# Kernel tuning notes

Measured on AMD Instinct MI355X. Metric: run time of the kernel, lower is better.

The kernel has to match this reference:

```python
import jax, jax.numpy as jnp
import numpy as np

NUM_NODES = 50000
NUM_RELS = 256
D = 256            # node_in_feat
TEXT_D = 256       # text_emb_dim
T_TOTAL = 24       # number of unique timestep graphs
E = 20000          # edges per timestep graph
B = 16             # batch of query times
SEQ_LEN = 7


def setup_inputs() -> dict:
    key = jax.random.key(0)
    ks = jax.random.split(key, 12)
    s = 1.0 / np.sqrt(D)
    return {
        "node_embeds": jax.random.normal(ks[0], (NUM_NODES, D), jnp.float32),
        "text_emb": jax.random.normal(ks[1], (T_TOTAL, E, TEXT_D), jnp.float32),
        "text_w_W": jax.random.uniform(ks[2], (TEXT_D, D), jnp.float32, -s, s),
        "text_w_b": jax.random.uniform(ks[3], (D,), jnp.float32, -s, s),
        "edge_w_W": jax.random.uniform(ks[4], (3 * D, D), jnp.float32, -s, s),
        "edge_w_b": jax.random.uniform(ks[5], (D,), jnp.float32, -s, s),
        "gru_Wih": jax.random.uniform(ks[6], (D, 3 * D), jnp.float32, -s, s),
        "gru_Whh": jax.random.uniform(ks[7], (D, 3 * D), jnp.float32, -s, s),
        "gru_bih": jax.random.uniform(ks[8], (3 * D,), jnp.float32, -s, s),
        "gru_bhh": jax.random.uniform(ks[9], (3 * D,), jnp.float32, -s, s),
        "edge_src": jax.random.randint(ks[10], (T_TOTAL, E), 0, NUM_NODES, jnp.int32),
        "edge_dst": jax.random.randint(jax.random.fold_in(ks[10], 1), (T_TOTAL, E), 0, NUM_NODES, jnp.int32),
        "edge_rel": jax.random.randint(jax.random.fold_in(ks[10], 2), (T_TOTAL, E), 0, NUM_RELS, jnp.int32),
        "time_idx": jax.random.randint(ks[11], (B, SEQ_LEN), 0, T_TOTAL, jnp.int32),
    }


def _gru(seqs, Wih, Whh, bih, bhh):
    # seqs: [B, R, S, d] -> run GRU over S, return final hidden [B, R, d]
    xs = jnp.moveaxis(seqs, 2, 0)  # [S, B, R, d]
    h0 = jnp.zeros(seqs.shape[:2] + (seqs.shape[-1],), seqs.dtype)

    def step(h, x):
        gi = x @ Wih + bih            # [B, R, 3d]
        gh = h @ Whh + bhh
        i_r, i_z, i_n = jnp.split(gi, 3, axis=-1)
        h_r, h_z, h_n = jnp.split(gh, 3, axis=-1)
        r = jax.nn.sigmoid(i_r + h_r)
        z = jax.nn.sigmoid(i_z + h_z)
        n = jnp.tanh(i_n + r * h_n)
        h_new = (1.0 - z) * n + z * h
        return h_new, None

    h_final, _ = jax.lax.scan(step, h0, xs)
    return h_final


def reference(node_embeds, text_emb, text_w_W, text_w_b, edge_w_W, edge_w_b,
              gru_Wih, gru_Whh, gru_bih, gru_bhh,
              edge_src, edge_dst, edge_rel, time_idx):
    # edge text projection (text_w): [T, E, D]
    text_h = text_emb @ text_w_W + text_w_b
    # gather node embeddings per edge endpoint
    h_src = node_embeds[edge_src]  # [T, E, D]
    h_dst = node_embeds[edge_dst]  # [T, E, D]
    # concat + edge MLP + ReLU: e_h = relu(edge_w([src || text || dst]))
    e = jnp.concatenate([h_src, text_h, h_dst], axis=-1)  # [T, E, 3D]
    e_h = jax.nn.relu(e @ edge_w_W + edge_w_b)            # [T, E, D]

    # scatter-mean of edge embeddings by relation type per timestep graph;
    # relations absent in a graph get zeros (init_rel_embeds = zeros)
    seg = lambda v, r: jax.ops.segment_sum(v, r, num_segments=NUM_RELS)
    sums = jax.vmap(seg)(e_h, edge_rel)                               # [T, R, D]
    counts = jax.vmap(seg)(jnp.ones(edge_rel.shape, e_h.dtype), edge_rel)  # [T, R]
    counts = counts[..., None]
    rel_emb = jnp.where(counts > 0, sums / jnp.maximum(counts, 1.0), 0.0)  # [T, R, D]

    # per query time: gather its window of timestep rel-embeddings and run
    # the GRU over time (relations act as the GRU batch dim, like transpose(0,1))
    seqs = rel_emb[time_idx]                 # [B, S, R, D]
    seqs = jnp.swapaxes(seqs, 1, 2)          # [B, R, S, D]
    hn = _gru(seqs, gru_Wih, gru_Whh, gru_bih, gru_bhh)  # [B, R, D]
    return hn
```

## Files before the change

### kernel.cpp

```cpp
#include <hip/hip_runtime.h>
#include <cstdint>
#include <cstddef>

#define NNODES 50000
#define NPAD   50048
#define NRELS  256
#define DIM    256
#define TT     24
#define EE     20000
#define BATCH  16
#define SEQQ   7

typedef __bf16 bf16;
typedef __bf16 bf16x4 __attribute__((ext_vector_type(4)));
typedef __bf16 bf16x8 __attribute__((ext_vector_type(8)));
typedef float  f32x4  __attribute__((ext_vector_type(4)));

__device__ __forceinline__ void gload16(const void* g, void* l){
  __builtin_amdgcn_global_load_lds((const __attribute__((address_space(1))) void*)g,
                                   (__attribute__((address_space(3))) void*)l, 16, 0, 0);
}


__global__ void k_cvt8(const float* __restrict__ in, bf16* __restrict__ out, int n8){
  int i = blockIdx.x*256 + threadIdx.x;
  if (i >= n8) return;
  const float4* p = (const float4*)in + (size_t)i*2;
  float4 a = p[0], b = p[1];
  bf16x8 o;
  o[0]=(bf16)a.x; o[1]=(bf16)a.y; o[2]=(bf16)a.z; o[3]=(bf16)a.w;
  o[4]=(bf16)b.x; o[5]=(bf16)b.y; o[6]=(bf16)b.z; o[7]=(bf16)b.w;
  ((bf16x8*)out)[i] = o;
}

__global__ void k_build_wbt(const float* __restrict__ tW, const float* __restrict__ eW,
                            bf16* __restrict__ WbT){
  int n = blockIdx.x, j = threadIdx.x;
  WbT[(size_t)n*768 + j]       = (bf16)eW[(size_t)j*256 + n];
  WbT[(size_t)n*768 + 512 + j] = (bf16)eW[(size_t)(512+j)*256 + n];
  float acc = 0.f;
  for (int m=0; m<256; ++m) acc += tW[(size_t)j*256 + m] * eW[(size_t)(256+m)*256 + n];
  WbT[(size_t)n*768 + 256 + j] = (bf16)acc;
}

__global__ void k_bias(const float* __restrict__ tb, const float* __restrict__ eW,
                       const float* __restrict__ eb, float* __restrict__ bf){
  int n = threadIdx.x;
  float acc = eb[n];
  for (int m=0; m<256; ++m) acc += tb[m] * eW[(size_t)(256+m)*256 + n];
  bf[n] = acc;
}

__global__ void k_gruWT(const float* __restrict__ W, bf16* __restrict__ WT){
  int n = blockIdx.x, k = threadIdx.x;
  WT[(size_t)n*256 + k] = (bf16)W[(size_t)k*768 + n];
}

__global__ void k_hist(const int* __restrict__ rel, int* __restrict__ counts,
                       int* __restrict__ offs, int* __restrict__ cursor){
  __shared__ int hist[256];
  __shared__ int scan[256];
  int t = blockIdx.x, tid = threadIdx.x;
  hist[tid] = 0;
  __syncthreads();
  for (int e = tid; e < EE; e += 256) atomicAdd(&hist[rel[(size_t)t*EE + e]], 1);
  __syncthreads();
  int v = hist[tid];
  scan[tid] = v;
  __syncthreads();
  for (int d=1; d<256; d<<=1){
    int add = (tid >= d) ? scan[tid-d] : 0;
    __syncthreads();
    scan[tid] += add;
    __syncthreads();
  }
  int ex = scan[tid] - v;
  counts[t*256+tid] = v;
  offs[t*256+tid]   = ex;
  cursor[t*256+tid] = ex;
}

__global__ void k_perm(const int* __restrict__ rel, const int* __restrict__ esrc,
                       const int* __restrict__ edst, int* __restrict__ cursor,
                       int* __restrict__ gperm, int* __restrict__ src_p,
                       int* __restrict__ dst_p, int* __restrict__ tr_p){
  int t = blockIdx.y;
  int e = blockIdx.x*256 + threadIdx.x;
  if (e < EE){
    int r = rel[(size_t)t*EE + e];
    int p = atomicAdd(&cursor[t*256 + r], 1);
    size_t g = (size_t)t*EE + p;
    gperm[g] = t*EE + e;
    src_p[g] = esrc[(size_t)t*EE + e];
    dst_p[g] = edst[(size_t)t*EE + e];
    tr_p[g]  = t*256 + r;
  }
}

__global__ __launch_bounds__(256) void k_projn(
    const bf16* __restrict__ Abf, const bf16* __restrict__ WbT, int koff,
    bf16* __restrict__ out)
{
  int m0 = blockIdx.x*128;
  int tid = threadIdx.x, lane = tid&63, w = tid>>6;
  int l15 = lane&15, lq = lane>>4;
  int c0 = w*64;
  __shared__ __align__(16) bf16 Al[128*32];
  __shared__ __align__(16) bf16 Bl[256*32];

  f32x4 acc[8][4];
  f32x4 z4 = {0.f,0.f,0.f,0.f};
  #pragma unroll
  for (int mi=0;mi<8;++mi)
    #pragma unroll
    for (int ni=0;ni<4;++ni) acc[mi][ni]=z4;

  for (int ks=0; ks<8; ++ks){
    int k0 = ks*32;
    #pragma unroll
    for (int p=0;p<2;++p){
      int c = p*256 + tid;
      int rw = c>>2, prt = c&3;
      int pp = prt ^ ((rw>>1)&3);
      const char* src = (const char*)(Abf + (size_t)(m0+rw)*256 + k0) + pp*16;
      gload16(src, (char*)Al + (size_t)(p*256 + w*64)*16);
    }
    #pragma unroll
    for (int p=0;p<4;++p){
      int c = p*256 + tid;
      int nn = c>>2, prt = c&3;
      int pp = prt ^ ((nn>>1)&3);
      const char* src = (const char*)(WbT + (size_t)nn*768 + koff + k0) + pp*16;
      gload16(src, (char*)Bl + (size_t)(p*256 + w*64)*16);
    }
    __syncthreads();
    bf16x8 b[4];
    #pragma unroll
    for (int ni=0;ni<4;++ni){
      int nn = c0 + ni*16 + l15;
      b[ni] = *(const bf16x8*)((const char*)Bl + (size_t)nn*64 + (size_t)((lq ^ ((nn>>1)&3))*16));
    }
    #pragma unroll
    for (int mi=0;mi<8;++mi){
      int rw = mi*16 + l15;
      bf16x8 a = *(const bf16x8*)((const char*)Al + (size_t)rw*64 + (size_t)((lq ^ ((rw>>1)&3))*16));
      #pragma unroll
      for (int ni=0;ni<4;++ni)
        acc[mi][ni] = __builtin_amdgcn_mfma_f32_16x16x32_bf16(b[ni], a, acc[mi][ni], 0,0,0);
    }
    __syncthreads();
  }
  #pragma unroll
  for (int mi=0;mi<8;++mi){
    int row = m0 + mi*16 + l15;
    #pragma unroll
    for (int ni=0;ni<4;++ni){
      bf16x4 o;
      #pragma unroll
      for (int q=0;q<4;++q) o[q] = (bf16)acc[mi][ni][q];
      *(bf16x4*)(out + (size_t)row*256 + c0 + ni*16 + lq*4) = o;
    }
  }
}

__global__ __launch_bounds__(256,3) void k_projtc(
    const float* __restrict__ text, const int* __restrict__ gperm,
    const bf16* __restrict__ WbT, const float* __restrict__ bfused,
    const bf16* __restrict__ P, const bf16* __restrict__ Q,
    const int* __restrict__ src_p, const int* __restrict__ dst_p,
    const int* __restrict__ tr_p, float* __restrict__ rel_sum)
{
  int m0 = blockIdx.x*64;
  int tid = threadIdx.x, lane = tid&63, w = tid>>6;
  int l15 = lane&15, lq = lane>>4;
  int c0 = w*64;
  __shared__ __align__(16) float Afl[3][64*32];
  __shared__ int trA[64], sIl[64], dIl[64];
  __shared__ int runS[65], runT[64];
  __shared__ int nRunS;

  if (tid < 64){
    int g = m0 + tid;
    trA[tid] = tr_p[g];
    sIl[tid] = src_p[g];
    dIl[tid] = dst_p[g];
  }
  __syncthreads();
  if (tid == 0){
    int nR = 0;
    for (int i=0;i<64;++i){
      if (i==0 || trA[i]!=trA[i-1]){ runS[nR]=i; runT[nR]=trA[i]; ++nR; }
    }
    runS[nR] = 64;
    nRunS = nR;
  }

  int rA0 = tid>>3;
  int partA = tid&7;
  int ppA = partA ^ (rA0 & 7);
  const float* aPtr0 = text + (size_t)gperm[m0 + rA0]*256      + ppA*4;
  const float* aPtr1 = text + (size_t)gperm[m0 + 32 + rA0]*256 + ppA*4;

  const bf16* bBase = WbT + (size_t)(c0 + l15)*768 + 256 + lq*8;

#define STAGEA(KS, BI)                                                        \
  { gload16(aPtr0 + (KS)*32, (char*)&Afl[BI][0] + (size_t)(w*64)*16);         \
    gload16(aPtr1 + (KS)*32, (char*)&Afl[BI][0] + (size_t)(256 + w*64)*16); }

#define LOADB(KS, DST)                                                        \
  { _Pragma("unroll")                                                         \
    for (int ni_=0;ni_<4;++ni_)                                               \
      DST[ni_] = *(const bf16x8*)(bBase + (size_t)ni_*16*768 + (KS)*32); }

  f32x4 acc[4][4];
  f32x4 z4 = {0.f,0.f,0.f,0.f};
  #pragma unroll
  for (int mi=0;mi<4;++mi)
    #pragma unroll
    for (int ni=0;ni<4;++ni) acc[mi][ni]=z4;

  bf16x8 bA[4], bB[4];
  STAGEA(0, 0);
  LOADB(0, bA);
  STAGEA(1, 1);

  #pragma unroll
  for (int ks=0; ks<8; ++ks){
    if (ks < 7){
      if ((ks & 1) == 0){ LOADB(ks+1, bB); } else { LOADB(ks+1, bA); }
    }
    if (ks < 6) STAGEA(ks+2, (ks+2)%3);
    if (ks < 6){
      asm volatile("s_waitcnt vmcnt(12)\n\ts_barrier" ::: "memory");
    } else if (ks == 6){
      asm volatile("s_waitcnt vmcnt(10)\n\ts_barrier" ::: "memory");
    } else {
      asm volatile("s_waitcnt vmcnt(4)\n\ts_barrier" ::: "memory");
    }
    __builtin_amdgcn_sched_barrier(0);
    bf16x8 a[4];
    #pragma unroll
    for (int mi=0;mi<4;++mi){
      int rw = mi*16 + l15;
      int sw = l15 & 7;
      const char* ab = (const char*)&Afl[ks%3][0] + (size_t)rw*128;
      f32x4 f0 = *(const f32x4*)(ab + (size_t)(((lq*2+0)^sw))*16);
      f32x4 f1 = *(const f32x4*)(ab + (size_t)(((lq*2+1)^sw))*16);
      bf16x8 o;
      o[0]=(bf16)f0[0]; o[1]=(bf16)f0[1]; o[2]=(bf16)f0[2]; o[3]=(bf16)f0[3];
      o[4]=(bf16)f1[0]; o[5]=(bf16)f1[1]; o[6]=(bf16)f1[2]; o[7]=(bf16)f1[3];
      a[mi] = o;
    }
    asm volatile("s_waitcnt lgkmcnt(0)" ::: "memory");
    __builtin_amdgcn_sched_barrier(0);
    if ((ks & 1) == 0){
      #pragma unroll
      for (int mi=0;mi<4;++mi)
        #pragma unroll
        for (int ni=0;ni<4;++ni)
          acc[mi][ni] = __builtin_amdgcn_mfma_f32_16x16x32_bf16(bA[ni], a[mi], acc[mi][ni], 0,0,0);
    } else {
      #pragma unroll
      for (int mi=0;mi<4;++mi)
        #pragma unroll
        for (int ni=0;ni<4;++ni)
          acc[mi][ni] = __builtin_amdgcn_mfma_f32_16x16x32_bf16(bB[ni], a[mi], acc[mi][ni], 0,0,0);
    }
    if (ks < 7)
      __builtin_amdgcn_s_barrier();
  }
#undef STAGEA
#undef LOADB

  float4 bias4[4];
  #pragma unroll
  for (int ni=0;ni<4;++ni)
    bias4[ni] = *(const float4*)(bfused + c0 + ni*16 + lq*4);

  #pragma unroll
  for (int mi=0;mi<4;++mi){
    int row = mi*16 + l15;
    int srow = sIl[row], drow = dIl[row];
    #pragma unroll
    for (int ni=0;ni<4;++ni){
      bf16x4 pv = *(const bf16x4*)(P + (size_t)srow*256 + c0 + ni*16 + lq*4);
      bf16x4 qv = *(const bf16x4*)(Q + (size_t)drow*256 + c0 + ni*16 + lq*4);
      f32x4 t4 = acc[mi][ni];
      t4[0] = fmaxf(t4[0] + (float)pv[0] + (float)qv[0] + bias4[ni].x, 0.f);
      t4[1] = fmaxf(t4[1] + (float)pv[1] + (float)qv[1] + bias4[ni].y, 0.f);
      t4[2] = fmaxf(t4[2] + (float)pv[2] + (float)qv[2] + bias4[ni].z, 0.f);
      t4[3] = fmaxf(t4[3] + (float)pv[3] + (float)qv[3] + bias4[ni].w, 0.f);
      acc[mi][ni] = t4;
    }
  }

  int nR = nRunS;
  for (int k=0; k<nR; ++k){
    int rs = runS[k], re = runS[k+1], tr = runT[k];
    float part16[16];
    #pragma unroll
    for (int ni=0;ni<4;++ni){
      #pragma unroll
      for (int q=0;q<4;++q){
        float s = 0.f;
        #pragma unroll
        for (int mi=0;mi<4;++mi){
          int row = mi*16 + l15;
          s += (row >= rs && row < re) ? acc[mi][ni][q] : 0.f;
        }
        part16[ni*4+q] = s;
      }
    }
    #pragma unroll
    for (int m=1; m<16; m<<=1){
      #pragma unroll
      for (int s=0;s<16;++s) part16[s] += __shfl_xor(part16[s], m);
    }
    float v = part16[0];
    #pragma unroll
    for (int s=1;s<16;++s) v = (l15==s) ? part16[s] : v;
    atomicAdd(&rel_sum[(size_t)tr*256 + c0 + ((l15>>2)<<4) + (lq<<2) + (l15&3)], v);
  }
}

__global__ void k_mean(const float* __restrict__ rel_sum, const int* __restrict__ counts,
                       bf16* __restrict__ rel_bf){
  int tr = blockIdx.x, c = threadIdx.x;
  int cnt = counts[tr];
  float v = (cnt > 0) ? rel_sum[(size_t)tr*256 + c] / (float)cnt : 0.f;
  rel_bf[(size_t)tr*256 + c] = (bf16)v;
}

__global__ __launch_bounds__(256) void k_gemm(
    const bf16* __restrict__ A, const bf16* __restrict__ BT,
    const float* __restrict__ bias, float* __restrict__ Out)
{
  int m0 = blockIdx.x*128, n0 = blockIdx.y*128;
  int tid = threadIdx.x, lane = tid&63, w = tid>>6;
  int l15 = lane&15, lq = lane>>4;
  __shared__ __align__(16) bf16 Al[128*32];
  __shared__ __align__(16) bf16 Bl[128*32];
  int wr = (w&1)*64, wc = (w>>1)*64;
  f32x4 acc[4][4];
  f32x4 z4 = {0.f,0.f,0.f,0.f};
  #pragma unroll
  for (int mi=0;mi<4;++mi)
    #pragma unroll
    for (int ni=0;ni<4;++ni) acc[mi][ni]=z4;
  for (int ks=0; ks<8; ++ks){
    int k0 = ks*32;
    #pragma unroll
    for (int p=0;p<2;++p){
      int c = p*256 + tid;
      int rw = c>>2, part = c&3;
      int pp = part ^ ((rw>>1)&3);
      const char* src = (const char*)(A + (size_t)(m0+rw)*256 + k0) + pp*16;
      gload16(src, (char*)Al + (size_t)(p*256 + w*64)*16);
    }
    #pragma unroll
    for (int p=0;p<2;++p){
      int c = p*256 + tid;
      int nn = c>>2, part = c&3;
      int pp = part ^ ((nn>>1)&3);
      const char* src = (const char*)(BT + (size_t)(n0+nn)*256 + k0) + pp*16;
      gload16(src, (char*)Bl + (size_t)(p*256 + w*64)*16);
    }
    __syncthreads();
    bf16x8 a[4], b[4];
    #pragma unroll
    for (int mi=0;mi<4;++mi){
      int rw = wr + mi*16 + l15;
      a[mi] = *(const bf16x8*)((const char*)Al + (size_t)rw*64 + (size_t)((lq ^ ((rw>>1)&3))*16));
    }
    #pragma unroll
    for (int ni=0;ni<4;++ni){
      int nn = wc + ni*16 + l15;
      b[ni] = *(const bf16x8*)((const char*)Bl + (size_t)nn*64 + (size_t)((lq ^ ((nn>>1)&3))*16));
    }
    #pragma unroll
    for (int mi=0;mi<4;++mi)
      #pragma unroll
      for (int ni=0;ni<4;++ni)
        acc[mi][ni] = __builtin_amdgcn_mfma_f32_16x16x32_bf16(a[mi], b[ni], acc[mi][ni], 0,0,0);
    __syncthreads();
  }
  #pragma unroll
  for (int ni=0;ni<4;++ni){
    int col = n0 + wc + ni*16 + l15;
    float bv = bias[col];
    #pragma unroll
    for (int mi=0;mi<4;++mi){
      #pragma unroll
      for (int q=0;q<4;++q){
        int row = m0 + wr + mi*16 + lq*4 + q;
        Out[(size_t)row*768 + col] = acc[mi][ni][q] + bv;
      }
    }
  }
}

__global__ __launch_bounds__(256) void k_gru(
    const float* __restrict__ GI, const bf16* __restrict__ WhhT,
    const float* __restrict__ bhh, const int* __restrict__ time_idx,
    float* __restrict__ out)
{
  int blk = blockIdx.x;
  int tid = threadIdx.x, lane = tid&63, w = tid>>6;
  int l15 = lane&15, lq = lane>>4;
  int b = blk >> 4;
  int rr = ((blk & 15)*16) + l15;
  __shared__ __align__(16) bf16 Ah[16*256];

  f32x4 h[4];
  #pragma unroll
  for (int jq=0;jq<4;++jq) h[jq] = f32x4{0.f,0.f,0.f,0.f};

  for (int s=0; s<SEQQ; ++s){
    int t = time_idx[b*SEQQ + s];
    size_t gib = (size_t)(t*256 + rr)*768;
    f32x4 gh[12];
    #pragma unroll
    for (int ni=0;ni<12;++ni){
      int col = (ni>>2)*256 + w*64 + (ni&3)*16 + lq*4;
      gh[ni] = *(const f32x4*)(bhh + col);
    }
    if (s > 0){
      #pragma unroll
      for (int ks=0; ks<8; ++ks){
        bf16x8 a = *(const bf16x8*)(&Ah[0] + (size_t)l15*256 + ks*32 + lq*8);
        #pragma unroll
        for (int ni=0;ni<12;++ni){
          int n = (ni>>2)*256 + w*64 + (ni&3)*16 + l15;
          bf16x8 wv = *(const bf16x8*)(WhhT + (size_t)n*256 + ks*32 + lq*8);
          gh[ni] = __builtin_amdgcn_mfma_f32_16x16x32_bf16(wv, a, gh[ni], 0,0,0);
        }
      }
    }
    #pragma unroll
    for (int jq=0;jq<4;++jq){
      int col = w*64 + jq*16 + lq*4;
      f32x4 ir = *(const f32x4*)(GI + gib + col);
      f32x4 iz = *(const f32x4*)(GI + gib + 256 + col);
      f32x4 in = *(const f32x4*)(GI + gib + 512 + col);
      #pragma unroll
      for (int q=0;q<4;++q){
        float rg = 1.f/(1.f + __expf(-(ir[q] + gh[jq][q])));
        float zz = 1.f/(1.f + __expf(-(iz[q] + gh[4+jq][q])));
        float nn = tanhf(in[q] + rg*gh[8+jq][q]);
        h[jq][q] = (1.f - zz)*nn + zz*h[jq][q];
      }
    }
    if (s < SEQQ-1){
      __syncthreads();
      #pragma unroll
      for (int jq=0;jq<4;++jq){
        bf16x4 o;
        #pragma unroll
        for (int q=0;q<4;++q) o[q] = (bf16)h[jq][q];
        *(bf16x4*)(&Ah[0] + (size_t)l15*256 + w*64 + jq*16 + lq*4) = o;
      }
      __syncthreads();
    }
  }
  #pragma unroll
  for (int jq=0;jq<4;++jq){
    f32x4 o = h[jq];
    *(f32x4*)(out + (size_t)(blk*16 + l15)*256 + w*64 + jq*16 + lq*4) = o;
  }
}

extern "C" void kernel_launch(void* const* d_in, const int* in_sizes, int n_in,
                              void* d_out, int out_size, void* d_ws, size_t ws_size,
                              hipStream_t stream)
{
  (void)in_sizes; (void)n_in; (void)out_size; (void)ws_size;
  const float* node_embeds = (const float*)d_in[0];
  const float* text_emb    = (const float*)d_in[1];
  const float* text_w_W    = (const float*)d_in[2];
  const float* text_w_b    = (const float*)d_in[3];
  const float* edge_w_W    = (const float*)d_in[4];
  const float* edge_w_b    = (const float*)d_in[5];
  const float* gru_Wih     = (const float*)d_in[6];
  const float* gru_Whh     = (const float*)d_in[7];
  const float* gru_bih     = (const float*)d_in[8];
  const float* gru_bhh     = (const float*)d_in[9];
  const int* edge_src      = (const int*)d_in[10];
  const int* edge_dst      = (const int*)d_in[11];
  const int* edge_rel      = (const int*)d_in[12];
  const int* time_idx      = (const int*)d_in[13];
  float* out = (float*)d_out;
  char* ws = (char*)d_ws;

  size_t o = 0;
  bf16*  WbT    = (bf16*) (ws + o); o += (size_t)768*256*2;
  bf16*  WihT   = (bf16*) (ws + o); o += (size_t)768*256*2;
  bf16*  WhhT   = (bf16*) (ws + o); o += (size_t)768*256*2;
  float* bfused = (float*)(ws + o); o += 1024;
  bf16*  node_bf= (bf16*) (ws + o); o += (size_t)NPAD*256*2;
  int*   counts = (int*)  (ws + o); o += (size_t)TT*256*4;
  int*   offs   = (int*)  (ws + o); o += (size_t)TT*256*4;
  int*   cursor = (int*)  (ws + o); o += (size_t)TT*256*4;
  int*   gperm  = (int*)  (ws + o); o += (size_t)TT*EE*4;
  int*   src_p  = (int*)  (ws + o); o += (size_t)TT*EE*4;
  int*   dst_p  = (int*)  (ws + o); o += (size_t)TT*EE*4;
  int*   tr_p   = (int*)  (ws + o); o += (size_t)TT*EE*4;
  bf16*  rel_bf = (bf16*) (ws + o); o += (size_t)TT*256*256*2;
  bf16*  P      = (bf16*) (ws + o); o += (size_t)NPAD*256*2;
  bf16*  Q      = (bf16*) (ws + o); o += (size_t)NPAD*256*2;
  float* rel_sum= (float*)(ws + o); o += (size_t)TT*256*256*4;
  float* GI     = (float*)(ws + o); o += (size_t)TT*256*768*4;

  k_cvt8<<<6250,256,0,stream>>>(node_embeds, node_bf, NNODES*256/8);
  k_build_wbt<<<256,256,0,stream>>>(text_w_W, edge_w_W, WbT);
  k_bias<<<1,256,0,stream>>>(text_w_b, edge_w_W, edge_w_b, bfused);
  k_gruWT<<<768,256,0,stream>>>(gru_Wih, WihT);
  k_gruWT<<<768,256,0,stream>>>(gru_Whh, WhhT);
  k_hist<<<TT,256,0,stream>>>(edge_rel, counts, offs, cursor);
  k_perm<<<dim3((EE+255)/256,TT),256,0,stream>>>(edge_rel, edge_src, edge_dst,
                                                 cursor, gperm, src_p, dst_p, tr_p);
  k_projn<<<NPAD/128,256,0,stream>>>(node_bf, WbT, 0,   P);
  k_projn<<<NPAD/128,256,0,stream>>>(node_bf, WbT, 512, Q);
  hipMemsetAsync(rel_sum, 0, (size_t)TT*256*256*4, stream);
  k_projtc<<<TT*EE/64,256,0,stream>>>(text_emb, gperm, WbT, bfused, P, Q,
                                      src_p, dst_p, tr_p, rel_sum);
  k_mean<<<TT*256,256,0,stream>>>(rel_sum, counts, rel_bf);
  k_gemm<<<dim3(48,6),256,0,stream>>>(rel_bf, WihT, gru_bih, GI);
  k_gru<<<256,256,0,stream>>>(GI, WhhT, gru_bhh, time_idx, out);
}
```

Before: 555.0 us.

## Load full text tile into LDS upfront instead of triple-buffered K pipeline

Replaces the 3-stage software-pipelined K loop, with its manual waitcnt and barrier choreography, in the text projection kernel. The kernel now issues all 16 global-to-LDS loads for the whole 64x256 fp32 text tile at once, then syncs a single time and runs the MFMA loop without barriers. B fragments are loaded directly each iteration. This needs 64KB of LDS per block, so the occupancy hint drops to 2 blocks per CU, and load latency is no longer overlapped with compute inside a block.

```diff
diff --git a/kernel.cpp b/kernel.cpp
--- a/kernel.cpp
+++ b/kernel.cpp
@@ -163,7 +163,7 @@
   }
 }
 
-__global__ __launch_bounds__(256,3) void k_projtc(
+__global__ __launch_bounds__(256,2) void k_projtc(
     const float* __restrict__ text, const int* __restrict__ gperm,
     const bf16* __restrict__ WbT, const float* __restrict__ bfused,
     const bf16* __restrict__ P, const bf16* __restrict__ Q,
@@ -174,13 +174,15 @@
   int tid = threadIdx.x, lane = tid&63, w = tid>>6;
   int l15 = lane&15, lq = lane>>4;
   int c0 = w*64;
-  __shared__ __align__(16) float Afl[3][64*32];
+  __shared__ __align__(16) float Afl[64*256];
+  __shared__ int gp[64];
   __shared__ int trA[64], sIl[64], dIl[64];
   __shared__ int runS[65], runT[64];
   __shared__ int nRunS;
 
   if (tid < 64){
     int g = m0 + tid;
+    gp[tid]  = gperm[g];
     trA[tid] = tr_p[g];
     sIl[tid] = src_p[g];
     dIl[tid] = dst_p[g];
@@ -195,22 +197,16 @@
     nRunS = nR;
   }
 
-  int rA0 = tid>>3;
-  int partA = tid&7;
-  int ppA = partA ^ (rA0 & 7);
-  const float* aPtr0 = text + (size_t)gperm[m0 + rA0]*256      + ppA*4;
-  const float* aPtr1 = text + (size_t)gperm[m0 + 32 + rA0]*256 + ppA*4;
+  #pragma unroll
+  for (int i=0;i<16;++i){
+    int ri = i*4 + w;
+    int sp = (lane & 56) | ((lane ^ ri) & 7);
+    const float* src = text + (size_t)gp[ri]*256 + sp*4;
+    gload16(src, (char*)Afl + (size_t)(i*256 + w*64)*16);
+  }
+  __syncthreads();
 
   const bf16* bBase = WbT + (size_t)(c0 + l15)*768 + 256 + lq*8;
-
-#define STAGEA(KS, BI)                                                        \
-  { gload16(aPtr0 + (KS)*32, (char*)&Afl[BI][0] + (size_t)(w*64)*16);         \
-    gload16(aPtr1 + (KS)*32, (char*)&Afl[BI][0] + (size_t)(256 + w*64)*16); }
-
-#define LOADB(KS, DST)                                                        \
-  { _Pragma("unroll")                                                         \
-    for (int ni_=0;ni_<4;++ni_)                                               \
-      DST[ni_] = *(const bf16x8*)(bBase + (size_t)ni_*16*768 + (KS)*32); }
 
   f32x4 acc[4][4];
   f32x4 z4 = {0.f,0.f,0.f,0.f};
@@ -219,58 +215,31 @@
     #pragma unroll
     for (int ni=0;ni<4;++ni) acc[mi][ni]=z4;
 
-  bf16x8 bA[4], bB[4];
-  STAGEA(0, 0);
-  LOADB(0, bA);
-  STAGEA(1, 1);
-
   #pragma unroll
   for (int ks=0; ks<8; ++ks){
-    if (ks < 7){
-      if ((ks & 1) == 0){ LOADB(ks+1, bB); } else { LOADB(ks+1, bA); }
-    }
-    if (ks < 6) STAGEA(ks+2, (ks+2)%3);
-    if (ks < 6){
-      asm volatile("s_waitcnt vmcnt(12)\n\ts_barrier" ::: "memory");
-    } else if (ks == 6){
-      asm volatile("s_waitcnt vmcnt(10)\n\ts_barrier" ::: "memory");
-    } else {
-      asm volatile("s_waitcnt vmcnt(4)\n\ts_barrier" ::: "memory");
-    }
-    __builtin_amdgcn_sched_barrier(0);
+    bf16x8 b[4];
+    #pragma unroll
+    for (int ni=0;ni<4;++ni)
+      b[ni] = *(const bf16x8*)(bBase + (size_t)ni*16*768 + ks*32);
     bf16x8 a[4];
     #pragma unroll
     for (int mi=0;mi<4;++mi){
       int rw = mi*16 + l15;
-      int sw = l15 & 7;
-      const char* ab = (const char*)&Afl[ks%3][0] + (size_t)rw*128;
-      f32x4 f0 = *(const f32x4*)(ab + (size_t)(((lq*2+0)^sw))*16);
-      f32x4 f1 = *(const f32x4*)(ab + (size_t)(((lq*2+1)^sw))*16);
+      int s7 = rw & 7;
+      const char* ab = (const char*)Afl + (size_t)rw*1024 + (size_t)ks*128;
+      f32x4 f0 = *(const f32x4*)(ab + (size_t)(((lq*2+0)^s7))*16);
+      f32x4 f1 = *(const f32x4*)(ab + (size_t)(((lq*2+1)^s7))*16);
       bf16x8 o;
       o[0]=(bf16)f0[0]; o[1]=(bf16)f0[1]; o[2]=(bf16)f0[2]; o[3]=(bf16)f0[3];
       o[4]=(bf16)f1[0]; o[5]=(bf16)f1[1]; o[6]=(bf16)f1[2]; o[7]=(bf16)f1[3];
       a[mi] = o;
     }
-    asm volatile("s_waitcnt lgkmcnt(0)" ::: "memory");
-    __builtin_amdgcn_sched_barrier(0);
-    if ((ks & 1) == 0){
-      #pragma unroll
-      for (int mi=0;mi<4;++mi)
-        #pragma unroll
-        for (int ni=0;ni<4;++ni)
-          acc[mi][ni] = __builtin_amdgcn_mfma_f32_16x16x32_bf16(bA[ni], a[mi], acc[mi][ni], 0,0,0);
-    } else {
-      #pragma unroll
-      for (int mi=0;mi<4;++mi)
-        #pragma unroll
-        for (int ni=0;ni<4;++ni)
-          acc[mi][ni] = __builtin_amdgcn_mfma_f32_16x16x32_bf16(bB[ni], a[mi], acc[mi][ni], 0,0,0);
-    }
-    if (ks < 7)
-      __builtin_amdgcn_s_barrier();
-  }
-#undef STAGEA
-#undef LOADB
+    #pragma unroll
+    for (int mi=0;mi<4;++mi)
+      #pragma unroll
+      for (int ni=0;ni<4;++ni)
+        acc[mi][ni] = __builtin_amdgcn_mfma_f32_16x16x32_bf16(b[ni], a[mi], acc[mi][ni], 0,0,0);
+  }
 
   float4 bias4[4];
   #pragma unroll
```

Measured after the change: 545.8 us. No clear change (-1.7%).
